# Optimization experiments

Hardware: AMD Instinct MI355X
Metric: run time of the kernel (lower is better)

Reference implementation:

```python
import jax, jax.numpy as jnp
import numpy as np

B, H, W, C, HID, V, EMB = 16, 24, 96, 1024, 256, 5000, 256
BN_EPS = 1e-5


def _lin(k, fin, fout, s=0.05):
    return jax.random.normal(k, (fin, fout), jnp.float32) * s


def setup_inputs():
    ks = jax.random.split(jax.random.key(0), 24)
    inp = {
        "input_y": jax.random.randint(ks[0], (B,), 0, V),
        "input_hidden": jax.random.normal(ks[1], (B, 1, HID), jnp.float32),
        "img_feature": jax.random.normal(ks[2], (B, C, H, W), jnp.float32),
        "feature_w": W,
        "attention_sum": jnp.zeros((B, 1, H, W), jnp.float32),
        "alpha_t": jax.random.uniform(ks[3], (B, 1, H, W), jnp.float32),
        "feature_h": H,
        "batch_size": B,
        "h_mask": jax.random.randint(ks[4], (B,), 1, H + 1),
        "w_mask": jax.random.randint(ks[5], (B,), 1, W + 1),
        "emb_table": jax.random.normal(ks[6], (V, EMB), jnp.float32) * 0.05,
        "gru1_wi": _lin(ks[7], EMB, 3 * HID), "gru1_wh": _lin(ks[8], HID, 3 * HID),
        "gru1_bi": jnp.zeros((3 * HID,), jnp.float32), "gru1_bh": jnp.zeros((3 * HID,), jnp.float32),
        "fc1_w": _lin(ks[9], HID, 256), "fc1_b": jnp.zeros((256,), jnp.float32),
        "gru2_wi": _lin(ks[10], C, 3 * HID), "gru2_wh": _lin(ks[11], HID, 3 * HID),
        "gru2_bi": jnp.zeros((3 * HID,), jnp.float32), "gru2_bh": jnp.zeros((3 * HID,), jnp.float32),
        "out_w": _lin(ks[12], 128, V), "out_b": jnp.zeros((V,), jnp.float32),
        "emb2_w": _lin(ks[13], 256, 128), "emb2_b": jnp.zeros((128,), jnp.float32),
        "conv1_w": jax.random.normal(ks[14], (1, 1, 3, 3), jnp.float32) * 0.05,
        "conv1_b": jnp.zeros((1,), jnp.float32),
        "conv_tan_w": jax.random.normal(ks[15], (256, 256, 3, 3), jnp.float32) * 0.02,
        "conv_tan_b": jnp.zeros((256,), jnp.float32),
        "fc2_w": _lin(ks[16], HID, 128), "fc2_b": jnp.zeros((128,), jnp.float32),
        "ua_w": _lin(ks[17], C, 256), "ua_b": jnp.zeros((256,), jnp.float32),
        "uf_w": _lin(ks[18], 1, 256), "uf_b": jnp.zeros((256,), jnp.float32),
        "v_w": _lin(ks[19], 256, 1), "v_b": jnp.zeros((1,), jnp.float32),
        "wc_w": _lin(ks[20], C, 128), "wc_b": jnp.zeros((128,), jnp.float32),
        "bn1_gamma": jnp.ones((256,), jnp.float32), "bn1_beta": jnp.zeros((256,), jnp.float32),
        "bn1_mean": jnp.zeros((256,), jnp.float32), "bn1_var": jnp.ones((256,), jnp.float32),
    }
    return inp


def _gru(x, h, wi, wh, bi, bh):
    # PyTorch GRUCell semantics
    gi = x @ wi + bi
    gh = h @ wh + bh
    ir, iz, inn = jnp.split(gi, 3, axis=-1)
    hr, hz, hn = jnp.split(gh, 3, axis=-1)
    r = jax.nn.sigmoid(ir + hr)
    z = jax.nn.sigmoid(iz + hz)
    n = jnp.tanh(inn + r * hn)
    return (1.0 - z) * n + z * h


def _conv(x, w, b):
    y = jax.lax.conv_general_dilated(x, w, (1, 1), 'SAME',
                                     dimension_numbers=('NCHW', 'OIHW', 'NCHW'))
    return y + b[None, :, None, None]


def reference(input_y, input_hidden, img_feature, feature_w, attention_sum, alpha_t,
              feature_h, batch_size, h_mask, w_mask,
              emb_table, gru1_wi, gru1_wh, gru1_bi, gru1_bh, fc1_w, fc1_b,
              gru2_wi, gru2_wh, gru2_bi, gru2_bh, out_w, out_b, emb2_w, emb2_b,
              conv1_w, conv1_b, conv_tan_w, conv_tan_b, fc2_w, fc2_b,
              ua_w, ua_b, uf_w, uf_b, v_w, v_b, wc_w, wc_b,
              bn1_gamma, bn1_beta, bn1_mean, bn1_var):
    b, c, h, w = img_feature.shape
    # per-sample validity mask over the feature map  [B, H, W]
    et_mask = ((jnp.arange(h)[None, :] < h_mask[:, None])[:, :, None]
               & (jnp.arange(w)[None, :] < w_mask[:, None])[:, None, :]).astype(jnp.float32)

    emb = emb_table[input_y]                      # [B, 256] (dropout = identity, eval)
    h0 = input_hidden[:, 0, :]                    # [B, HID]
    st1 = _gru(emb, h0, gru1_wi, gru1_wh, gru1_bi, gru1_bh)
    st1 = st1 @ fc1_w + fc1_b                     # [B, 256]

    alpha_c = _conv(alpha_t, conv1_w, conv1_b)    # [B, 1, H, W]
    att_sum = attention_sum + alpha_c             # coverage accumulator

    img1 = jnp.einsum('bchw,cd->bhwd', img_feature, ua_w) + ua_b  # [B,H,W,256]
    att1 = att_sum[:, 0, :, :, None] * uf_w[0] + uf_b             # Linear(1,256)
    et = st1[:, None, None, :] + img1 + att1      # [B, H, W, 256]

    et_nchw = jnp.transpose(et, (0, 3, 1, 2))
    et_nchw = _conv(et_nchw, conv_tan_w, conv_tan_b)
    et_nchw = et_nchw * et_mask[:, None]
    inv = bn1_gamma / jnp.sqrt(bn1_var + BN_EPS)  # eval-mode BatchNorm2d(256)
    et_nchw = (et_nchw - bn1_mean[None, :, None, None]) * inv[None, :, None, None] \
              + bn1_beta[None, :, None, None]
    et_nchw = jnp.tanh(et_nchw)

    e = jnp.einsum('bchw,c->bhw', et_nchw, v_w[:, 0]) + v_b[0]    # [B, H, W]
    e_exp = jnp.exp(e) * et_mask
    e_sum = jnp.sum(e_exp, axis=(1, 2))
    alpha = e_exp / (e_sum[:, None, None] + 1e-8)                 # masked softmax

    ct = jnp.einsum('bhw,bchw->bc', alpha, img_feature)           # [B, 1024]
    st = _gru(ct, st1, gru2_wi, gru2_wh, gru2_bi, gru2_bh)        # [B, HID]
    hidden_next = st[:, None, :]

    pre = (st @ fc2_w + fc2_b) + (emb @ emb2_w + emb2_b) + (ct @ wc_w + wc_b)  # [B,128]
    output = jax.nn.log_softmax(pre @ out_w + out_b, axis=1)[:, None, :]       # [B,1,V]
    return output, hidden_next, alpha[:, None], att_sum
```

## Files before the change

kernel.cpp:

```cpp
#include <hip/hip_runtime.h>
#include <hip/hip_bf16.h>

#define B   16
#define H   24
#define W   96
#define C   1024
#define HID 256
#define V   5000
#define EMB 256
#define HW  (H*W)
#define BN_EPS 1e-5f
#define H2  (H+2)
#define W2  (W+2)

#define OUT0 0
#define OUT1 (B*V)
#define OUT2 (OUT1 + B*HID)
#define OUT3 (OUT2 + B*HW)

#define WSB_IMGT  0
#define WSB_ETP   75497472
#define WSB_WTB   96370688
#define WSB_UAT   97550336
#define WSB_E     98074624
#define WSB_ST1   98369536
#define WSB_CT    98385920
#define WSB_PRE   98451456
#define WSB_GIGH1 98459648
#define WSB_GH2   98574336
#define WSB_GI2   98631680

typedef __attribute__((ext_vector_type(8))) short short8;
typedef __attribute__((ext_vector_type(4))) float f32x4;

__device__ inline unsigned short f2bf(float f) {
    union { float f; unsigned int u; } v; v.f = f;
    unsigned int r = v.u + 0x7fffu + ((v.u >> 16) & 1u);
    return (unsigned short)(r >> 16);
}
__device__ inline float bf2f(unsigned short u) {
    union { unsigned int u; float f; } v; v.u = ((unsigned int)u) << 16;
    return v.f;
}

__device__ inline void gload_lds16(const unsigned short* g, unsigned short* l) {
    __builtin_amdgcn_global_load_lds(
        (const __attribute__((address_space(1))) void*)g,
        (__attribute__((address_space(3))) void*)l,
        16, 0, 0);
}

__global__ __launch_bounds__(256) void k_imgT(const float* img, unsigned short* imgT)
{
    int hw0 = blockIdx.x*64, c0 = blockIdx.y*128, b = blockIdx.z;
    int t = threadIdx.x;
    __shared__ __align__(16) unsigned short tr[64*256];
    int row = t & 63;
    int sgb = t >> 6;
    const float* src = img + ((size_t)b*C + c0)*HW + hw0 + row;
    #pragma unroll
    for (int k = 0; k < 4; ++k) {
        int sg = sgb + k*4;
        union { short8 v; unsigned short u[8]; } pk;
        #pragma unroll
        for (int j = 0; j < 8; ++j)
            pk.u[j] = f2bf(src[(size_t)(sg*8 + j)*HW]);
        *(short8*)&tr[row*256 + (sg ^ (row & 31))*8] = pk.v;
    }
    __syncthreads();
    #pragma unroll
    for (int k = 0; k < 4; ++k) {
        int i = k*256 + t;
        int orow = i >> 4, sg = i & 15;
        *(short8*)&imgT[((size_t)(b*HW) + hw0 + orow)*1024 + c0 + sg*8] =
            *(const short8*)&tr[orow*256 + (sg ^ (orow & 31))*8];
    }
}

__global__ __launch_bounds__(256) void k_prep(
    const float* conv_w_src, unsigned short* wtb,
    const float* ua_w, unsigned short* uat,
    const float* att_in, const float* alpha_t, const float* cw, const float* cb, float* att_out,
    float* ct, unsigned short* et_p)
{
    int x = blockIdx.x, t = threadIdx.x;
    if (x < 2304) {
        int idx = x*256 + t;
        int c = idx & 255; int o = (idx >> 8) & 255; int khw = idx >> 16;
        wtb[(khw*256 + o)*256 + c] = f2bf(conv_w_src[(o*256 + c)*9 + khw]);
    } else if (x < 3328) {
        int idx = (x - 2304)*256 + t;
        int c = idx & 1023; int d = idx >> 10;
        uat[d*1024 + c] = f2bf(ua_w[c*256 + d]);
    } else if (x < 3472) {
        int i = (x - 3328)*256 + t;
        int w = i % W; int h = (i / W) % H; int b = i / HW;
        float s = cb[0];
        #pragma unroll
        for (int kh = 0; kh < 3; ++kh) {
            int r = h + kh - 1; if (r < 0 || r >= H) continue;
            #pragma unroll
            for (int kw = 0; kw < 3; ++kw) {
                int c = w + kw - 1; if (c < 0 || c >= W) continue;
                s += alpha_t[(b*H + r)*W + c]*cw[kh*3+kw];
            }
        }
        att_out[i] = att_in[i] + s;
    } else if (x < 3536) {
        ct[(x - 3472)*256 + t] = 0.f;
    } else {
        int flat = (x - 3536)*256 + t;
        int b = flat / 7808; int r = flat - b*7808;
        int h2, w2, j;
        if (r < 3136)      { h2 = 0;  w2 = r >> 5;          j = r & 31; }
        else if (r < 6272) { h2 = 25; w2 = (r - 3136) >> 5; j = (r - 3136) & 31; }
        else {
            int rr = r - 6272;
            h2 = 1 + (rr >> 6);
            int s = rr & 63;
            w2 = (s < 32) ? 0 : 97;
            j = s & 31;
        }
        ((int4*)et_p)[((size_t)(b*H2 + h2)*W2 + w2)*32 + j] = make_int4(0,0,0,0);
    }
}

__global__ __launch_bounds__(256) void k_tail1(
    const int* y, const float* emb_table, const float* h0,
    const float* wi, const float* wh, float* gigh)
{
    int virt = blockIdx.x*16;
    int t = threadIdx.x;
    bool gi_mode = virt < 768;
    __shared__ float a_l[16*256];
    for (int i = t; i < 4096; i += 256) {
        int b = i >> 8, k = i & 255;
        a_l[i] = gi_mode ? emb_table[y[b]*EMB + k] : h0[b*HID + k];
    }
    __syncthreads();
    int nl = t & 15, b = t >> 4;
    int n = (gi_mode ? virt : virt - 768) + nl;
    const float* wp = gi_mode ? wi : wh;
    float acc = 0.f;
    #pragma unroll 16
    for (int k = 0; k < 256; ++k) acc += a_l[b*256 + k]*wp[k*768 + n];
    gigh[b*1536 + virt + nl] = acc;
}

__global__ __launch_bounds__(256) void k_fc1c(
    const float* gigh, const float* h0, const float* bi, const float* bh,
    const float* fc1_w, const float* fc1_b, float* st1)
{
    int n0 = blockIdx.x*16, t = threadIdx.x;
    __shared__ float a_l[16*256];
    for (int i = t; i < 4096; i += 256) {
        int b = i >> 8, k = i & 255;
        const float* g = gigh + b*1536;
        float ir = g[k] + bi[k], iz = g[256+k] + bi[256+k], in_ = g[512+k] + bi[512+k];
        float hr = g[768+k] + bh[k], hz = g[1024+k] + bh[256+k], hn = g[1280+k] + bh[512+k];
        float r = 1.f/(1.f+__expf(-(ir+hr)));
        float z = 1.f/(1.f+__expf(-(iz+hz)));
        float n = tanhf(in_ + r*hn);
        a_l[i] = (1.f - z)*n + z*h0[b*HID + k];
    }
    __syncthreads();
    int nl = t & 15, b = t >> 4;
    float acc = fc1_b[n0+nl];
    #pragma unroll 16
    for (int k = 0; k < 256; ++k) acc += a_l[b*256+k]*fc1_w[k*256 + n0 + nl];
    st1[b*256 + n0 + nl] = acc;
}

__global__ __launch_bounds__(256, 3) void k_et(
    const unsigned short* imgT, const unsigned short* uat, const float* ua_b,
    const float* st1, const float* att_sum, const float* uf_w, const float* uf_b,
    unsigned short* et_p)
{
    int h = blockIdx.x, ny = blockIdx.y, b = blockIdx.z;
    int t = threadIdx.x;
    int wv = t >> 6, lane = t & 63, q = lane >> 4, ln = lane & 15;
    int wm = wv & 1, wn = wv >> 1;
    int n0 = ny*128 + wn*64;
    __shared__ __align__(16) unsigned short a_l[2*1536*8];

    f32x4 acc[12];
    #pragma unroll
    for (int i = 0; i < 12; ++i) acc[i] = (f32x4){0.f,0.f,0.f,0.f};

    const unsigned short* ab = imgT + ((size_t)(b*HW) + h*W)*1024;
    const unsigned short* bbase = uat + (size_t)(n0 + ln)*1024 + q*8;

    int ebase[3];
    #pragma unroll
    for (int mf = 0; mf < 3; ++mf) {
        int m = wm*48 + ln + 16*mf;
        ebase[mf] = m*128 + (q ^ (m & 7))*8;
    }

    int goff[6], loff[6];
    #pragma unroll
    for (int it = 0; it < 6; ++it) {
        int L = it*256 + t;
        int m = L >> 4, s = L & 15;
        goff[it] = m*1024 + (s ^ (m & 7))*8;
        loff[it] = (it*256 + wv*64)*8;
    }

    #pragma unroll
    for (int it = 0; it < 6; ++it)
        gload_lds16(ab + goff[it], &a_l[loff[it]]);
    __syncthreads();

    int cur = 0;
    for (int c0 = 0; c0 < 1024; c0 += 128) {
        int bufS = cur*12288, nbufS = bufS ^ 12288;
        if (c0 < 896) {
            #pragma unroll
            for (int it = 0; it < 6; ++it)
                gload_lds16(ab + goff[it] + c0 + 128, &a_l[nbufS + loff[it]]);
        }
        #pragma unroll
        for (int cs = 0; cs < 128; cs += 32) {
            short8 av[3];
            #pragma unroll
            for (int mf = 0; mf < 3; ++mf)
                av[mf] = *(const short8*)&a_l[bufS + (ebase[mf] ^ cs)];
            #pragma unroll
            for (int j = 0; j < 4; ++j) {
                short8 bv = *(const short8*)(bbase + (size_t)(j*16)*1024 + c0 + cs);
                #pragma unroll
                for (int mf = 0; mf < 3; ++mf)
                    acc[mf*4+j] = __builtin_amdgcn_mfma_f32_16x16x32_bf16(av[mf], bv, acc[mf*4+j], 0, 0, 0);
            }
        }
        __syncthreads();
        cur ^= 1;
    }

    float att_m[12];
    #pragma unroll
    for (int mf = 0; mf < 3; ++mf)
        #pragma unroll
        for (int r = 0; r < 4; ++r)
            att_m[mf*4+r] = att_sum[(b*H + h)*W + wm*48 + mf*16 + q*4 + r];
    #pragma unroll
    for (int j = 0; j < 4; ++j) {
        int n = n0 + j*16 + ln;
        float s1 = st1[b*256 + n] + ua_b[n];
        float ufw = uf_w[n], ufb = uf_b[n];
        #pragma unroll
        for (int mf = 0; mf < 3; ++mf)
            #pragma unroll
            for (int r = 0; r < 4; ++r) {
                int m = wm*48 + mf*16 + q*4 + r;
                float v = acc[mf*4+j][r] + s1 + att_m[mf*4+r]*ufw + ufb;
                et_p[((size_t)(b*H2 + h + 1)*W2 + (m + 1))*256 + n] = f2bf(v);
            }
    }
}

__global__ __launch_bounds__(256, 3) void k_conv(
    const unsigned short* et_p, const unsigned short* wtb, const float* cb,
    const float* bn_g, const float* bn_b, const float* bn_m, const float* bn_v,
    const float* v_w, float* e_part)
{
    int h = blockIdx.x, ny = blockIdx.y, b = blockIdx.z;
    int t = threadIdx.x;
    int wv = t >> 6, lane = t & 63, q = lane >> 4, ln = lane & 15;
    int wm = wv & 1, wn = wv >> 1;
    int n0 = ny*128 + wn*64;
    __shared__ __align__(16) unsigned short patch[2*1176*8];
    __shared__ float lds_red[2][96];

    f32x4 acc[12];
    #pragma unroll
    for (int i = 0; i < 12; ++i) acc[i] = (f32x4){0.f,0.f,0.f,0.f};

    int abase[3][3];
    #pragma unroll
    for (int mf = 0; mf < 3; ++mf)
        #pragma unroll
        for (int kw = 0; kw < 3; ++kw) {
            int x2 = wm*48 + ln + 16*mf + kw;
            abase[mf][kw] = x2*32 + (q ^ ((x2 >> 1) & 3))*8;
        }

    const unsigned short* gb = et_p + (size_t)(b*H2 + h)*W2*256;
    const unsigned short* wb = wtb + (size_t)(n0 + ln)*256 + q*8;

    int goff[5], loff[5]; bool act[5];
    #pragma unroll
    for (int it = 0; it < 5; ++it) {
        int L = it*256 + t;
        act[it] = L < 1176;
        int Lc = act[it] ? L : 0;
        int pl = Lc / 392; int rem = Lc - pl*392;
        int x2 = rem >> 2, s = rem & 3;
        goff[it] = (pl*W2 + x2)*256 + (s ^ ((x2 >> 1) & 3))*8;
        loff[it] = (it*256 + wv*64)*8;
    }

    #pragma unroll
    for (int it = 0; it < 5; ++it)
        if (act[it]) gload_lds16(gb + goff[it], &patch[loff[it]]);
    __syncthreads();

    int cur = 0;
    for (int cc = 0; cc < 8; ++cc) {
        int bufS = cur*9408, nbufS = bufS ^ 9408;
        if (cc < 7) {
            int c1 = (cc + 1)*32;
            #pragma unroll
            for (int it = 0; it < 5; ++it)
                if (act[it]) gload_lds16(gb + goff[it] + c1, &patch[nbufS + loff[it]]);
        }
        int c0 = cc*32;
        #pragma unroll
        for (int kh = 0; kh < 3; ++kh) {
            #pragma unroll
            for (int kw = 0; kw < 3; ++kw) {
                short8 av[3];
                #pragma unroll
                for (int mf = 0; mf < 3; ++mf)
                    av[mf] = *(const short8*)&patch[bufS + kh*3136 + abase[mf][kw]];
                const unsigned short* brow = wb + (size_t)(kh*3 + kw)*65536 + c0;
                #pragma unroll
                for (int j = 0; j < 4; ++j) {
                    short8 bv = *(const short8*)(brow + j*4096);
                    #pragma unroll
                    for (int mf = 0; mf < 3; ++mf)
                        acc[mf*4+j] = __builtin_amdgcn_mfma_f32_16x16x32_bf16(av[mf], bv, acc[mf*4+j], 0, 0, 0);
                }
            }
        }
        __syncthreads();
        cur ^= 1;
    }

    float psum[12];
    #pragma unroll
    for (int i = 0; i < 12; ++i) psum[i] = 0.f;
    #pragma unroll
    for (int j = 0; j < 4; ++j) {
        int o = n0 + j*16 + ln;
        float inv  = bn_g[o]*rsqrtf(bn_v[o] + BN_EPS);
        float mean = bn_m[o], beta = bn_b[o], bias = cb[o], vw = v_w[o];
        #pragma unroll
        for (int mf = 0; mf < 3; ++mf)
            #pragma unroll
            for (int r = 0; r < 4; ++r) {
                float x = (acc[mf*4+j][r] + bias - mean)*inv + beta;
                x = fminf(fmaxf(x, -15.f), 15.f);
                float ex = __expf(2.f*x);
                psum[mf*4+r] += ((ex - 1.f)/(ex + 1.f))*vw;
            }
    }
    #pragma unroll
    for (int s = 1; s < 16; s <<= 1)
        #pragma unroll
        for (int i = 0; i < 12; ++i) psum[i] += __shfl_xor(psum[i], s);
    if (ln == 0) {
        #pragma unroll
        for (int mf = 0; mf < 3; ++mf)
            #pragma unroll
            for (int r = 0; r < 4; ++r)
                lds_red[wn][wm*48 + mf*16 + q*4 + r] = psum[mf*4+r];
    }
    __syncthreads();
    if (t < 96)
        e_part[(size_t)ny*(B*HW) + (b*H + h)*W + t] = lds_red[0][t] + lds_red[1][t];
}

__global__ __launch_bounds__(256) void k_softmax(
    const float* e_part, const int* h_mask, const int* w_mask, const float* v_b,
    float* alpha_out)
{
    int b = blockIdx.x, t = threadIdx.x;
    int hm = h_mask[b], wm = w_mask[b];
    float vb = v_b[0];
    __shared__ float red[256];
    float vals[9];
    float loc = 0.f;
    #pragma unroll
    for (int i = 0; i < 9; ++i) {
        int hw = t + i*256;
        int hh = hw / W, ww = hw % W;
        float v = 0.f;
        if (hh < hm && ww < wm)
            v = __expf(e_part[b*HW + hw] + e_part[B*HW + b*HW + hw] + vb);
        vals[i] = v; loc += v;
    }
    red[t] = loc; __syncthreads();
    for (int s = 128; s > 0; s >>= 1) { if (t < s) red[t] += red[t+s]; __syncthreads(); }
    float inv = 1.f/(red[0] + 1e-8f);
    #pragma unroll
    for (int i = 0; i < 9; ++i) alpha_out[b*HW + t + i*256] = vals[i]*inv;
}

__global__ __launch_bounds__(256) void k_ct(
    const float* alpha, const unsigned short* imgT, float* ct)
{
    int s = blockIdx.x, b = blockIdx.y, t = threadIdx.x;
    int cg = (t & 127)*8, half = t >> 7;
    float acc[8];
    #pragma unroll
    for (int j = 0; j < 8; ++j) acc[j] = 0.f;
    for (int i = 0; i < 72; ++i) {
        int hw = s*144 + i*2 + half;
        float a = alpha[b*HW + hw];
        union { short8 v; unsigned short u[8]; } pk;
        pk.v = *(const short8*)&imgT[((size_t)(b*HW) + hw)*1024 + cg];
        #pragma unroll
        for (int j = 0; j < 8; ++j) acc[j] += a*bf2f(pk.u[j]);
    }
    #pragma unroll
    for (int j = 0; j < 8; ++j) atomicAdd(&ct[b*1024 + cg + j], acc[j]);
}

__global__ __launch_bounds__(256) void k_g2(
    const float* st1, const int* y, const float* emb_table,
    const float* wh, const float* emb2_w, float* gh2,
    const float* ct, const float* wi, const float* wc_w, float* gi2p)
{
    int x = blockIdx.x, t = threadIdx.x;
    __shared__ float a_l[16*256];
    if (x < 56) {
        int virt = x*16;
        bool ghm = virt < 768;
        for (int i = t; i < 4096; i += 256) {
            int b = i >> 8, k = i & 255;
            a_l[i] = ghm ? st1[b*256 + k] : emb_table[y[b]*EMB + k];
        }
        __syncthreads();
        int nl = t & 15, b = t >> 4;
        float acc = 0.f;
        if (ghm) {
            int n = virt + nl;
            #pragma unroll 16
            for (int k = 0; k < 256; ++k) acc += a_l[b*256+k]*wh[k*768 + n];
        } else {
            int n = virt - 768 + nl;
            #pragma unroll 16
            for (int k = 0; k < 256; ++k) acc += a_l[b*256+k]*emb2_w[k*128 + n];
        }
        gh2[b*896 + virt + nl] = acc;
    } else {
        int xx = x - 56;
        int ks = xx / 56, virt = (xx - ks*56)*16;
        int k0 = ks*256;
        for (int i = t; i < 4096; i += 256) {
            int b = i >> 8, k = i & 255;
            a_l[i] = ct[b*1024 + k0 + k];
        }
        __syncthreads();
        int nl = t & 15, b = t >> 4;
        float acc = 0.f;
        if (virt < 768) {
            int n = virt + nl;
            #pragma unroll 16
            for (int k = 0; k < 256; ++k) acc += a_l[b*256+k]*wi[(k0+k)*768 + n];
        } else {
            int n = virt - 768 + nl;
            #pragma unroll 16
            for (int k = 0; k < 256; ++k) acc += a_l[b*256+k]*wc_w[(k0+k)*128 + n];
        }
        gi2p[(ks*16 + b)*896 + virt + nl] = acc;
    }
}

__global__ __launch_bounds__(256) void k_fc2c(
    const float* gi2p, const float* gh2, const float* st1,
    const float* bi, const float* bh,
    const float* fc2_w, const float* fc2_b, const float* emb2_b, const float* wc_b,
    float* hidden_out, float* pre)
{
    int n0 = blockIdx.x*16, t = threadIdx.x;
    __shared__ float st_l[16*256];
    for (int i = t; i < 4096; i += 256) {
        int b = i >> 8, k = i & 255;
        float ir = bi[k], iz = bi[256+k], in_ = bi[512+k];
        #pragma unroll
        for (int ks = 0; ks < 4; ++ks) {
            const float* g = gi2p + (ks*16 + b)*896;
            ir += g[k]; iz += g[256+k]; in_ += g[512+k];
        }
        const float* gh = gh2 + b*896;
        float hr = gh[k] + bh[k], hz = gh[256+k] + bh[256+k], hn = gh[512+k] + bh[512+k];
        float h = st1[b*256+k];
        float r = 1.f/(1.f+__expf(-(ir+hr)));
        float z = 1.f/(1.f+__expf(-(iz+hz)));
        float n = tanhf(in_ + r*hn);
        float s = (1.f - z)*n + z*h;
        st_l[i] = s;
        if (blockIdx.x == 0) hidden_out[b*HID + k] = s;
    }
    __syncthreads();
    int nl = t & 15, b = t >> 4;
    int n = n0 + nl;
    float acc = fc2_b[n] + emb2_b[n] + wc_b[n] + gh2[b*896 + 768 + n];
    #pragma unroll
    for (int ks = 0; ks < 4; ++ks) acc += gi2p[(ks*16 + b)*896 + 768 + n];
    #pragma unroll 16
    for (int k = 0; k < 256; ++k) acc += st_l[b*256+k]*fc2_w[k*128 + n];
    pre[b*128 + n] = acc;
}

__global__ __launch_bounds__(256) void k_logits(
    const float* pre, const float* out_w, const float* out_b, float* out)
{
    int j0 = blockIdx.x*64, t = threadIdx.x;
    __shared__ float pre_l[16*128];
    for (int i = t; i < 2048; i += 256) pre_l[i] = pre[i];
    __syncthreads();
    int jl = t & 63, bg = t >> 6;
    int j = j0 + jl;
    if (j >= V) return;
    float acc0=0.f, acc1=0.f, acc2=0.f, acc3=0.f;
    const float* pl = pre_l + bg*4*128;
    #pragma unroll 8
    for (int k = 0; k < 128; ++k) {
        float wv = out_w[k*V + j];
        acc0 += pl[k]*wv; acc1 += pl[128+k]*wv; acc2 += pl[256+k]*wv; acc3 += pl[384+k]*wv;
    }
    float ob = out_b[j];
    out[(bg*4+0)*V + j] = acc0 + ob;
    out[(bg*4+1)*V + j] = acc1 + ob;
    out[(bg*4+2)*V + j] = acc2 + ob;
    out[(bg*4+3)*V + j] = acc3 + ob;
}

__global__ __launch_bounds__(1024) void k_lsm(float* out)
{
    int b = blockIdx.x, t = threadIdx.x;
    __shared__ float red[1024];
    float lg[5]; float mx = -1e30f;
    #pragma unroll
    for (int i = 0; i < 5; ++i) {
        int j = t + i*1024;
        lg[i] = (j < V) ? out[b*V + j] : -1e30f;
        mx = fmaxf(mx, lg[i]);
    }
    red[t] = mx; __syncthreads();
    for (int s = 512; s > 0; s >>= 1) { if (t < s) red[t] = fmaxf(red[t], red[t+s]); __syncthreads(); }
    float gmax = red[0]; __syncthreads();
    float se = 0.f;
    #pragma unroll
    for (int i = 0; i < 5; ++i) { int j = t + i*1024; if (j < V) se += __expf(lg[i] - gmax); }
    red[t] = se; __syncthreads();
    for (int s = 512; s > 0; s >>= 1) { if (t < s) red[t] += red[t+s]; __syncthreads(); }
    float lse = logf(red[0]);
    #pragma unroll
    for (int i = 0; i < 5; ++i) { int j = t + i*1024; if (j < V) out[b*V + j] = lg[i] - gmax - lse; }
}

extern "C" void kernel_launch(void* const* d_in, const int* in_sizes, int n_in,
                              void* d_out, int out_size, void* d_ws, size_t ws_size,
                              hipStream_t stream)
{
    const int*   input_y      = (const int*)  d_in[0];
    const float* input_hidden = (const float*)d_in[1];
    const float* img          = (const float*)d_in[2];
    const float* attention    = (const float*)d_in[4];
    const float* alpha_t      = (const float*)d_in[5];
    const int*   h_mask       = (const int*)  d_in[8];
    const int*   w_mask       = (const int*)  d_in[9];
    const float* emb_table    = (const float*)d_in[10];
    const float* gru1_wi      = (const float*)d_in[11];
    const float* gru1_wh      = (const float*)d_in[12];
    const float* gru1_bi      = (const float*)d_in[13];
    const float* gru1_bh      = (const float*)d_in[14];
    const float* fc1_w        = (const float*)d_in[15];
    const float* fc1_b        = (const float*)d_in[16];
    const float* gru2_wi      = (const float*)d_in[17];
    const float* gru2_wh      = (const float*)d_in[18];
    const float* gru2_bi      = (const float*)d_in[19];
    const float* gru2_bh      = (const float*)d_in[20];
    const float* out_w        = (const float*)d_in[21];
    const float* out_b        = (const float*)d_in[22];
    const float* emb2_w       = (const float*)d_in[23];
    const float* emb2_b       = (const float*)d_in[24];
    const float* conv1_w      = (const float*)d_in[25];
    const float* conv1_b      = (const float*)d_in[26];
    const float* conv_tan_w   = (const float*)d_in[27];
    const float* conv_tan_b   = (const float*)d_in[28];
    const float* fc2_w        = (const float*)d_in[29];
    const float* fc2_b        = (const float*)d_in[30];
    const float* ua_w         = (const float*)d_in[31];
    const float* ua_b         = (const float*)d_in[32];
    const float* uf_w         = (const float*)d_in[33];
    const float* uf_b         = (const float*)d_in[34];
    const float* v_w          = (const float*)d_in[35];
    const float* v_b          = (const float*)d_in[36];
    const float* wc_w         = (const float*)d_in[37];
    const float* wc_b         = (const float*)d_in[38];
    const float* bn1_gamma    = (const float*)d_in[39];
    const float* bn1_beta     = (const float*)d_in[40];
    const float* bn1_mean     = (const float*)d_in[41];
    const float* bn1_var      = (const float*)d_in[42];

    float* out = (float*)d_out;
    char*  ws  = (char*)d_ws;
    unsigned short* imgT = (unsigned short*)(ws + WSB_IMGT);
    unsigned short* et_p = (unsigned short*)(ws + WSB_ETP);
    unsigned short* wtb  = (unsigned short*)(ws + WSB_WTB);
    unsigned short* uat  = (unsigned short*)(ws + WSB_UAT);
    float* e_part = (float*)(ws + WSB_E);
    float* st1   = (float*)(ws + WSB_ST1);
    float* ct    = (float*)(ws + WSB_CT);
    float* pre   = (float*)(ws + WSB_PRE);
    float* gigh1 = (float*)(ws + WSB_GIGH1);
    float* gh2   = (float*)(ws + WSB_GH2);
    float* gi2p  = (float*)(ws + WSB_GI2);

    float* out_logits = out + OUT0;
    float* out_hidden = out + OUT1;
    float* out_alpha  = out + OUT2;
    float* out_attsum = out + OUT3;

    k_imgT<<<dim3(HW/64, C/128, B), 256, 0, stream>>>(img, imgT);
    k_prep<<<4024, 256, 0, stream>>>(conv_tan_w, wtb, ua_w, uat,
                                     attention, alpha_t, conv1_w, conv1_b, out_attsum,
                                     ct, et_p);
    k_tail1<<<96, 256, 0, stream>>>(input_y, emb_table, input_hidden,
                                    gru1_wi, gru1_wh, gigh1);
    k_fc1c<<<16, 256, 0, stream>>>(gigh1, input_hidden, gru1_bi, gru1_bh,
                                   fc1_w, fc1_b, st1);
    k_et<<<dim3(H, 2, B), 256, 0, stream>>>(imgT, uat, ua_b, st1, out_attsum,
                                            uf_w, uf_b, et_p);
    k_conv<<<dim3(H, 2, B), 256, 0, stream>>>(et_p, wtb, conv_tan_b,
                                              bn1_gamma, bn1_beta, bn1_mean, bn1_var,
                                              v_w, e_part);
    k_softmax<<<B, 256, 0, stream>>>(e_part, h_mask, w_mask, v_b, out_alpha);
    k_ct<<<dim3(16, B), 256, 0, stream>>>(out_alpha, imgT, ct);
    k_g2<<<280, 256, 0, stream>>>(st1, input_y, emb_table, gru2_wh, emb2_w, gh2,
                                  ct, gru2_wi, wc_w, gi2p);
    k_fc2c<<<8, 256, 0, stream>>>(gi2p, gh2, st1, gru2_bi, gru2_bh,
                                  fc2_w, fc2_b, emb2_b, wc_b, out_hidden, pre);
    k_logits<<<(V + 63)/64, 256, 0, stream>>>(pre, out_w, out_b, out_logits);
    k_lsm<<<B, 1024, 0, stream>>>(out_logits);
}
```

Measured before the change: 604.6 us.

## Split et and conv GEMM tiles by half-width and spread ct over more blocks

The et and conv MFMA kernels now give each block half a row (48 pixels), and each wave covers 32 output channels instead of a 48x64 tile. This doubles the grid to 1536 blocks, halves LDS and accumulator registers, and raises the launch-bounds occupancy hint from 3 to 6. The LDS swizzles and the load mapping are rewritten to fit the smaller tiles. The ct reduction grid grows from 16 to 64 blocks per batch, which raises atomicAdd traffic. Smaller tiles lower per-block data reuse: neighbouring blocks fetch more weight and overlapping halo data.

New measurement: 661.0 us. 9.3% more time.

```diff
diff --git a/kernel.cpp b/kernel.cpp
--- a/kernel.cpp
+++ b/kernel.cpp
@@ -171,52 +171,54 @@
     st1[b*256 + n0 + nl] = acc;
 }
 
-__global__ __launch_bounds__(256, 3) void k_et(
+__global__ __launch_bounds__(256, 6) void k_et(
     const unsigned short* imgT, const unsigned short* uat, const float* ua_b,
     const float* st1, const float* att_sum, const float* uf_w, const float* uf_b,
     unsigned short* et_p)
 {
-    int h = blockIdx.x, ny = blockIdx.y, b = blockIdx.z;
+    int hb = blockIdx.x; int h = hb >> 1, mh = hb & 1;
+    int ny = blockIdx.y, b = blockIdx.z;
     int t = threadIdx.x;
     int wv = t >> 6, lane = t & 63, q = lane >> 4, ln = lane & 15;
-    int wm = wv & 1, wn = wv >> 1;
-    int n0 = ny*128 + wn*64;
-    __shared__ __align__(16) unsigned short a_l[2*1536*8];
-
-    f32x4 acc[12];
-    #pragma unroll
-    for (int i = 0; i < 12; ++i) acc[i] = (f32x4){0.f,0.f,0.f,0.f};
-
-    const unsigned short* ab = imgT + ((size_t)(b*HW) + h*W)*1024;
+    int n0 = ny*128 + wv*32;
+    __shared__ __align__(16) unsigned short a_l[2*6144];
+
+    f32x4 acc[6];
+    #pragma unroll
+    for (int i = 0; i < 6; ++i) acc[i] = (f32x4){0.f,0.f,0.f,0.f};
+
+    const unsigned short* ab = imgT + ((size_t)(b*HW) + h*W + mh*48)*1024;
     const unsigned short* bbase = uat + (size_t)(n0 + ln)*1024 + q*8;
 
     int ebase[3];
     #pragma unroll
     for (int mf = 0; mf < 3; ++mf) {
-        int m = wm*48 + ln + 16*mf;
+        int m = ln + 16*mf;
         ebase[mf] = m*128 + (q ^ (m & 7))*8;
     }
 
-    int goff[6], loff[6];
-    #pragma unroll
-    for (int it = 0; it < 6; ++it) {
-        int L = it*256 + t;
+    int goff[3], loff[3];
+    #pragma unroll
+    for (int it = 0; it < 3; ++it) {
+        int g = wv + it*4;
+        int L = g*64 + lane;
         int m = L >> 4, s = L & 15;
-        goff[it] = m*1024 + (s ^ (m & 7))*8;
-        loff[it] = (it*256 + wv*64)*8;
-    }
-
-    #pragma unroll
-    for (int it = 0; it < 6; ++it)
+        int sig = (s & 8) | ((s ^ m) & 7);
+        goff[it] = m*1024 + sig*8;
+        loff[it] = g*512;
+    }
+
+    #pragma unroll
+    for (int it = 0; it < 3; ++it)
         gload_lds16(ab + goff[it], &a_l[loff[it]]);
     __syncthreads();
 
     int cur = 0;
     for (int c0 = 0; c0 < 1024; c0 += 128) {
-        int bufS = cur*12288, nbufS = bufS ^ 12288;
+        int bufS = cur*6144, nbufS = bufS ^ 6144;
         if (c0 < 896) {
             #pragma unroll
-            for (int it = 0; it < 6; ++it)
+            for (int it = 0; it < 3; ++it)
                 gload_lds16(ab + goff[it] + c0 + 128, &a_l[nbufS + loff[it]]);
         }
         #pragma unroll
@@ -226,11 +228,11 @@
             for (int mf = 0; mf < 3; ++mf)
                 av[mf] = *(const short8*)&a_l[bufS + (ebase[mf] ^ cs)];
             #pragma unroll
-            for (int j = 0; j < 4; ++j) {
+            for (int j = 0; j < 2; ++j) {
                 short8 bv = *(const short8*)(bbase + (size_t)(j*16)*1024 + c0 + cs);
                 #pragma unroll
                 for (int mf = 0; mf < 3; ++mf)
-                    acc[mf*4+j] = __builtin_amdgcn_mfma_f32_16x16x32_bf16(av[mf], bv, acc[mf*4+j], 0, 0, 0);
+                    acc[mf*2+j] = __builtin_amdgcn_mfma_f32_16x16x32_bf16(av[mf], bv, acc[mf*2+j], 0, 0, 0);
             }
         }
         __syncthreads();
@@ -242,9 +244,9 @@
     for (int mf = 0; mf < 3; ++mf)
         #pragma unroll
         for (int r = 0; r < 4; ++r)
-            att_m[mf*4+r] = att_sum[(b*H + h)*W + wm*48 + mf*16 + q*4 + r];
-    #pragma unroll
-    for (int j = 0; j < 4; ++j) {
+            att_m[mf*4+r] = att_sum[(b*H + h)*W + mh*48 + mf*16 + q*4 + r];
+    #pragma unroll
+    for (int j = 0; j < 2; ++j) {
         int n = n0 + j*16 + ln;
         float s1 = st1[b*256 + n] + ua_b[n];
         float ufw = uf_w[n], ufb = uf_b[n];
@@ -252,67 +254,68 @@
         for (int mf = 0; mf < 3; ++mf)
             #pragma unroll
             for (int r = 0; r < 4; ++r) {
-                int m = wm*48 + mf*16 + q*4 + r;
-                float v = acc[mf*4+j][r] + s1 + att_m[mf*4+r]*ufw + ufb;
+                int m = mh*48 + mf*16 + q*4 + r;
+                float v = acc[mf*2+j][r] + s1 + att_m[mf*4+r]*ufw + ufb;
                 et_p[((size_t)(b*H2 + h + 1)*W2 + (m + 1))*256 + n] = f2bf(v);
             }
     }
 }
 
-__global__ __launch_bounds__(256, 3) void k_conv(
+__global__ __launch_bounds__(256, 6) void k_conv(
     const unsigned short* et_p, const unsigned short* wtb, const float* cb,
     const float* bn_g, const float* bn_b, const float* bn_m, const float* bn_v,
     const float* v_w, float* e_part)
 {
-    int h = blockIdx.x, ny = blockIdx.y, b = blockIdx.z;
+    int hb = blockIdx.x; int h = hb >> 1, mh = hb & 1;
+    int ny = blockIdx.y, b = blockIdx.z;
     int t = threadIdx.x;
     int wv = t >> 6, lane = t & 63, q = lane >> 4, ln = lane & 15;
-    int wm = wv & 1, wn = wv >> 1;
-    int n0 = ny*128 + wn*64;
-    __shared__ __align__(16) unsigned short patch[2*1176*8];
-    __shared__ float lds_red[2][96];
-
-    f32x4 acc[12];
-    #pragma unroll
-    for (int i = 0; i < 12; ++i) acc[i] = (f32x4){0.f,0.f,0.f,0.f};
+    int n0 = ny*128 + wv*32;
+    __shared__ __align__(16) unsigned short patch[2*4800];
+    __shared__ float lds_red[4][48];
+
+    f32x4 acc[6];
+    #pragma unroll
+    for (int i = 0; i < 6; ++i) acc[i] = (f32x4){0.f,0.f,0.f,0.f};
 
     int abase[3][3];
     #pragma unroll
     for (int mf = 0; mf < 3; ++mf)
         #pragma unroll
         for (int kw = 0; kw < 3; ++kw) {
-            int x2 = wm*48 + ln + 16*mf + kw;
-            abase[mf][kw] = x2*32 + (q ^ ((x2 >> 1) & 3))*8;
-        }
-
-    const unsigned short* gb = et_p + (size_t)(b*H2 + h)*W2*256;
+            int x2 = ln + 16*mf + kw;
+            abase[mf][kw] = x2*32 + (q ^ (x2 & 3))*8;
+        }
+
+    const unsigned short* gb = et_p + ((size_t)(b*H2 + h)*W2 + mh*48)*256;
     const unsigned short* wb = wtb + (size_t)(n0 + ln)*256 + q*8;
 
-    int goff[5], loff[5]; bool act[5];
-    #pragma unroll
-    for (int it = 0; it < 5; ++it) {
-        int L = it*256 + t;
-        act[it] = L < 1176;
-        int Lc = act[it] ? L : 0;
-        int pl = Lc / 392; int rem = Lc - pl*392;
+    int goff[3], loff[3]; bool la[3];
+    #pragma unroll
+    for (int it = 0; it < 3; ++it) {
+        int g = wv + it*4;
+        int L = g*64 + lane;
+        la[it] = (g < 10) && (L < 600);
+        int Lc = la[it] ? L : 0;
+        int pl = Lc / 200; int rem = Lc - pl*200;
         int x2 = rem >> 2, s = rem & 3;
-        goff[it] = (pl*W2 + x2)*256 + (s ^ ((x2 >> 1) & 3))*8;
-        loff[it] = (it*256 + wv*64)*8;
-    }
-
-    #pragma unroll
-    for (int it = 0; it < 5; ++it)
-        if (act[it]) gload_lds16(gb + goff[it], &patch[loff[it]]);
+        goff[it] = (pl*W2 + x2)*256 + (s ^ (x2 & 3))*8;
+        loff[it] = g*512;
+    }
+
+    #pragma unroll
+    for (int it = 0; it < 3; ++it)
+        if (la[it]) gload_lds16(gb + goff[it], &patch[loff[it]]);
     __syncthreads();
 
     int cur = 0;
     for (int cc = 0; cc < 8; ++cc) {
-        int bufS = cur*9408, nbufS = bufS ^ 9408;
+        int bufS = cur*4800, nbufS = bufS ^ 4800;
         if (cc < 7) {
             int c1 = (cc + 1)*32;
             #pragma unroll
-            for (int it = 0; it < 5; ++it)
-                if (act[it]) gload_lds16(gb + goff[it] + c1, &patch[nbufS + loff[it]]);
+            for (int it = 0; it < 3; ++it)
+                if (la[it]) gload_lds16(gb + goff[it] + c1, &patch[nbufS + loff[it]]);
         }
         int c0 = cc*32;
         #pragma unroll
@@ -322,14 +325,14 @@
                 short8 av[3];
                 #pragma unroll
                 for (int mf = 0; mf < 3; ++mf)
-                    av[mf] = *(const short8*)&patch[bufS + kh*3136 + abase[mf][kw]];
+                    av[mf] = *(const short8*)&patch[bufS + kh*1600 + abase[mf][kw]];
                 const unsigned short* brow = wb + (size_t)(kh*3 + kw)*65536 + c0;
                 #pragma unroll
-                for (int j = 0; j < 4; ++j) {
+                for (int j = 0; j < 2; ++j) {
                     short8 bv = *(const short8*)(brow + j*4096);
                     #pragma unroll
                     for (int mf = 0; mf < 3; ++mf)
-                        acc[mf*4+j] = __builtin_amdgcn_mfma_f32_16x16x32_bf16(av[mf], bv, acc[mf*4+j], 0, 0, 0);
+                        acc[mf*2+j] = __builtin_amdgcn_mfma_f32_16x16x32_bf16(av[mf], bv, acc[mf*2+j], 0, 0, 0);
                 }
             }
         }
@@ -341,7 +344,7 @@
     #pragma unroll
     for (int i = 0; i < 12; ++i) psum[i] = 0.f;
     #pragma unroll
-    for (int j = 0; j < 4; ++j) {
+    for (int j = 0; j < 2; ++j) {
         int o = n0 + j*16 + ln;
         float inv  = bn_g[o]*rsqrtf(bn_v[o] + BN_EPS);
         float mean = bn_m[o], beta = bn_b[o], bias = cb[o], vw = v_w[o];
@@ -349,7 +352,7 @@
         for (int mf = 0; mf < 3; ++mf)
             #pragma unroll
             for (int r = 0; r < 4; ++r) {
-                float x = (acc[mf*4+j][r] + bias - mean)*inv + beta;
+                float x = (acc[mf*2+j][r] + bias - mean)*inv + beta;
                 x = fminf(fmaxf(x, -15.f), 15.f);
                 float ex = __expf(2.f*x);
                 psum[mf*4+r] += ((ex - 1.f)/(ex + 1.f))*vw;
@@ -364,11 +367,12 @@
         for (int mf = 0; mf < 3; ++mf)
             #pragma unroll
             for (int r = 0; r < 4; ++r)
-                lds_red[wn][wm*48 + mf*16 + q*4 + r] = psum[mf*4+r];
-    }
-    __syncthreads();
-    if (t < 96)
-        e_part[(size_t)ny*(B*HW) + (b*H + h)*W + t] = lds_red[0][t] + lds_red[1][t];
+                lds_red[wv][mf*16 + q*4 + r] = psum[mf*4+r];
+    }
+    __syncthreads();
+    if (t < 48)
+        e_part[(size_t)ny*(B*HW) + (b*H + h)*W + mh*48 + t] =
+            lds_red[0][t] + lds_red[1][t] + lds_red[2][t] + lds_red[3][t];
 }
 
 __global__ __launch_bounds__(256) void k_softmax(
@@ -405,8 +409,8 @@
     float acc[8];
     #pragma unroll
     for (int j = 0; j < 8; ++j) acc[j] = 0.f;
-    for (int i = 0; i < 72; ++i) {
-        int hw = s*144 + i*2 + half;
+    for (int i = 0; i < 18; ++i) {
+        int hw = s*36 + i*2 + half;
         float a = alpha[b*HW + hw];
         union { short8 v; unsigned short u[8]; } pk;
         pk.v = *(const short8*)&imgT[((size_t)(b*HW) + hw)*1024 + cg];
@@ -625,13 +629,13 @@
                                     gru1_wi, gru1_wh, gigh1);
     k_fc1c<<<16, 256, 0, stream>>>(gigh1, input_hidden, gru1_bi, gru1_bh,
                                    fc1_w, fc1_b, st1);
-    k_et<<<dim3(H, 2, B), 256, 0, stream>>>(imgT, uat, ua_b, st1, out_attsum,
-                                            uf_w, uf_b, et_p);
-    k_conv<<<dim3(H, 2, B), 256, 0, stream>>>(et_p, wtb, conv_tan_b,
-                                              bn1_gamma, bn1_beta, bn1_mean, bn1_var,
-                                              v_w, e_part);
+    k_et<<<dim3(H*2, 2, B), 256, 0, stream>>>(imgT, uat, ua_b, st1, out_attsum,
+                                              uf_w, uf_b, et_p);
+    k_conv<<<dim3(H*2, 2, B), 256, 0, stream>>>(et_p, wtb, conv_tan_b,
+                                                bn1_gamma, bn1_beta, bn1_mean, bn1_var,
+                                                v_w, e_part);
     k_softmax<<<B, 256, 0, stream>>>(e_part, h_mask, w_mask, v_b, out_alpha);
-    k_ct<<<dim3(16, B), 256, 0, stream>>>(out_alpha, imgT, ct);
+    k_ct<<<dim3(64, B), 256, 0, stream>>>(out_alpha, imgT, ct);
     k_g2<<<280, 256, 0, stream>>>(st1, input_y, emb_table, gru2_wh, emb2_w, gh2,
                                   ct, gru2_wi, wc_w, gi2p);
     k_fc2c<<<8, 256, 0, stream>>>(gi2p, gh2, st1, gru2_bi, gru2_bh,
```
